# Optimization experiments

Measured on AMD Instinct MI355X. Metric: run time of the kernel, lower is better.

Reference implementation:

```python
import jax, jax.numpy as jnp
import numpy as np

B, T, C = 4, 1024, 1024
H, D = 16, 64


def setup_inputs() -> dict:
    key = jax.random.key(0)
    ks = jax.random.split(key, 5)
    sc = 0.02
    x = jax.random.normal(ks[0], (B, T, C), dtype=jnp.float32)
    Wq = jax.random.normal(ks[1], (H, C, D), dtype=jnp.float32) * sc
    Wk = jax.random.normal(ks[2], (H, C, D), dtype=jnp.float32) * sc
    Wv = jax.random.normal(ks[3], (H, C, D), dtype=jnp.float32) * sc
    Wp = jax.random.normal(ks[4], (H * D, C), dtype=jnp.float32) * sc
    bp = jnp.zeros((C,), dtype=jnp.float32)
    return {"x": x, "Wq": Wq, "Wk": Wk, "Wv": Wv, "Wp": Wp, "bp": bp}


def reference(x, Wq, Wk, Wv, Wp, bp):
    # per-head projections (bias-free, as in nanoGPT Head)
    q = jnp.einsum('btc,hcd->bhtd', x, Wq)
    k = jnp.einsum('btc,hcd->bhtd', x, Wk)
    v = jnp.einsum('btc,hcd->bhtd', x, Wv)
    scale = 1.0 / jnp.sqrt(jnp.asarray(D, dtype=x.dtype))
    scores = jnp.einsum('bhtd,bhsd->bhts', q, k) * scale  # [B,H,T,T]
    causal = jnp.tril(jnp.ones((T, T), dtype=bool))
    scores = jnp.where(causal, scores, jnp.asarray(-jnp.inf, dtype=scores.dtype))
    attn = jax.nn.softmax(scores, axis=-1)
    out = jnp.einsum('bhts,bhsd->bhtd', attn, v)  # [B,H,T,D]
    out = out.transpose(0, 2, 1, 3).reshape(B, T, H * D)  # concat heads
    return out @ Wp + bp  # final projection (dropout=0)
```

## Files before the change

kernel.cpp:

```cpp
#include <hip/hip_runtime.h>
#include <hip/hip_bf16.h>

typedef unsigned short u16;
typedef __bf16 bf16x8 __attribute__((ext_vector_type(8)));
typedef float floatx4 __attribute__((ext_vector_type(4)));

#define SB 4
#define ST 1024
#define SC 1024
#define SH 16
#define SD 64

__device__ __forceinline__ u16 f2bf(float f) {
    unsigned int u = __builtin_bit_cast(unsigned int, f);
    u += 0x7fffu + ((u >> 16) & 1u);
    return (u16)(u >> 16);
}

__device__ __forceinline__ void gload16(const u16* g, u16* l) {
    __builtin_amdgcn_global_load_lds(
        (const __attribute__((address_space(1))) unsigned int*)g,
        (__attribute__((address_space(3))) unsigned int*)l, 16, 0, 0);
}

__global__ void k_prep(const float* __restrict__ x,
                       const float* __restrict__ Wq, const float* __restrict__ Wk,
                       const float* __restrict__ Wv, const float* __restrict__ Wp,
                       u16* __restrict__ xb, u16* __restrict__ Wqkv, u16* __restrict__ Wpt) {
    __shared__ float tile[64 * 65];
    const int id = blockIdx.x, tid = threadIdx.x;
    if (id < 4096) {
        int i = id * 256 + tid;
        float4 v = ((const float4*)x)[i];
        uint2 o;
        o.x = (unsigned)f2bf(v.x) | ((unsigned)f2bf(v.y) << 16);
        o.y = (unsigned)f2bf(v.z) | ((unsigned)f2bf(v.w) << 16);
        ((uint2*)xb)[i] = o;
    } else if (id < 4864) {
        const int id1 = id - 4096;
        const int qkv = id1 >> 8, rem = id1 & 255, h = rem >> 4, c0 = (rem & 15) * 64;
        const float* src = qkv == 0 ? Wq : (qkv == 1 ? Wk : Wv);
        #pragma unroll
        for (int i = 0; i < 16; ++i) {
            int idx = tid + i * 256;
            int r = idx >> 6, d = idx & 63;
            tile[r * 65 + d] = src[(h * SC + c0 + r) * SD + d];
        }
        __syncthreads();
        #pragma unroll
        for (int i = 0; i < 16; ++i) {
            int idx = tid + i * 256;
            int d = idx >> 6, cc = idx & 63;
            Wqkv[(qkv * 1024 + h * SD + d) * SC + c0 + cc] = f2bf(tile[cc * 65 + d]);
        }
    } else {
        const int id2 = id - 4864;
        const int n0 = (id2 & 15) * 64, k0 = (id2 >> 4) * 64;
        #pragma unroll
        for (int i = 0; i < 16; ++i) {
            int idx = tid + i * 256;
            int r = idx >> 6, nn = idx & 63;
            tile[r * 65 + nn] = Wp[(k0 + r) * SC + n0 + nn];
        }
        __syncthreads();
        #pragma unroll
        for (int i = 0; i < 16; ++i) {
            int idx = tid + i * 256;
            int nr = idx >> 6, kk = idx & 63;
            Wpt[(n0 + nr) * (SH * SD) + k0 + kk] = f2bf(tile[kk * 65 + nr]);
        }
    }
}

__launch_bounds__(256)
__global__ void k_gemm(const u16* __restrict__ A, const u16* __restrict__ Bt,
                       int M, int N, int K,
                       u16* __restrict__ Qb, u16* __restrict__ Kb, u16* __restrict__ Vt) {
    constexpr int BM = 128, BN = 128, SM = 4, SN = 4;
    __shared__ u16 Als[BM * 64];
    __shared__ u16 Bls[BN * 64];
    const int tid = threadIdx.x, lane = tid & 63, w = tid >> 6;
    const int quad = lane >> 4, l16 = lane & 15;
    const int sr = lane >> 3, sc = lane & 7;
    const int nt = N / BN;
    const int m0 = (blockIdx.x / nt) * BM, n0 = (blockIdx.x % nt) * BN;
    const int wm = (w >> 1) * 64, wn = (w & 1) * 64;

    floatx4 acc[SM][SN] = {};
    const int niter = K / 64;
    for (int it = 0; it < niter; ++it) {
        const int k0 = it * 64;
        #pragma unroll
        for (int i = 0; i < 4; ++i) {
            int rb = (w * 4 + i) * 8;
            gload16(&A[(long)(m0 + rb + sr) * K + k0 + ((sc ^ sr) << 3)], &Als[rb * 64]);
            gload16(&Bt[(long)(n0 + rb + sr) * K + k0 + ((sc ^ sr) << 3)], &Bls[rb * 64]);
        }
        __syncthreads();
        bf16x8 af[SM][2], bfr[SN][2];
        #pragma unroll
        for (int sm = 0; sm < SM; ++sm) {
            int row = wm + sm * 16 + l16;
            #pragma unroll
            for (int ks = 0; ks < 2; ++ks)
                af[sm][ks] = *(const bf16x8*)&Als[row * 64 + (((ks * 4 + quad) ^ (row & 7)) << 3)];
        }
        #pragma unroll
        for (int sn = 0; sn < SN; ++sn) {
            int row = wn + sn * 16 + l16;
            #pragma unroll
            for (int ks = 0; ks < 2; ++ks)
                bfr[sn][ks] = *(const bf16x8*)&Bls[row * 64 + (((ks * 4 + quad) ^ (row & 7)) << 3)];
        }
        #pragma unroll
        for (int ks = 0; ks < 2; ++ks)
            #pragma unroll
            for (int sm = 0; sm < SM; ++sm)
                #pragma unroll
                for (int sn = 0; sn < SN; ++sn)
                    acc[sm][sn] = __builtin_amdgcn_mfma_f32_16x16x32_bf16(bfr[sn][ks], af[sm][ks], acc[sm][sn], 0, 0, 0);
        if (it + 1 < niter) __syncthreads();
    }
    const int qkv = n0 >> 10;
    const float qs = qkv == 0 ? 0.18033688011112042f : 1.0f;
    #pragma unroll
    for (int sm = 0; sm < SM; ++sm) {
        const int m = m0 + wm + sm * 16 + l16;
        const int bb = m >> 10, t = m & 1023;
        #pragma unroll
        for (int sn = 0; sn < SN; ++sn) {
            const int dl = (n0 & 1023) + wn + sn * 16 + (quad << 2);
            const int h = dl >> 6, d0 = dl & 63;
            u16 pk[4];
            #pragma unroll
            for (int r = 0; r < 4; ++r) pk[r] = f2bf(acc[sm][sn][r] * qs);
            if (qkv == 2) {
                const long vb = (long)(bb * SH + h) * SD * ST + t;
                #pragma unroll
                for (int r = 0; r < 4; ++r) Vt[vb + (long)(d0 + r) * ST] = pk[r];
            } else {
                u16* dst = qkv == 0 ? Qb : Kb;
                *(uint2*)&dst[(((long)(bb * SH + h) * ST + t) << 6) + d0] = *(uint2*)pk;
            }
        }
    }
}

__launch_bounds__(256)
__global__ void k_oproj(const u16* __restrict__ A, const u16* __restrict__ Bt,
                        const float* __restrict__ bias, float* __restrict__ Cout) {
    constexpr int K = 1024, N = 1024;
    __shared__ u16 Als[4][64 * 64];
    __shared__ u16 Bls[4][64 * 64];
    const int tid = threadIdx.x, lane = tid & 63, w = tid >> 6;
    const int quad = lane >> 4, l16 = lane & 15;
    const int sr = lane >> 3, sc = lane & 7;
    const int m0 = (blockIdx.x >> 4) * 64, n0 = (blockIdx.x & 15) * 64;
    const int wm = (w >> 1) * 32, wn = (w & 1) * 32;

    floatx4 acc[2][2] = {};
    for (int kb = 0; kb < 4; ++kb) {
        const int k0 = kb * 256;
        #pragma unroll
        for (int seg = 0; seg < 4; ++seg) {
            #pragma unroll
            for (int i = 0; i < 2; ++i) {
                int rb = (w * 2 + i) * 8;
                gload16(&A[(long)(m0 + rb + sr) * K + k0 + seg * 64 + ((sc ^ sr) << 3)], &Als[seg][rb * 64]);
                gload16(&Bt[(long)(n0 + rb + sr) * K + k0 + seg * 64 + ((sc ^ sr) << 3)], &Bls[seg][rb * 64]);
            }
        }
        __syncthreads();
        #pragma unroll
        for (int seg = 0; seg < 4; ++seg) {
            bf16x8 af[2][2], bfr[2][2];
            #pragma unroll
            for (int sm = 0; sm < 2; ++sm) {
                int row = wm + sm * 16 + l16;
                #pragma unroll
                for (int ks = 0; ks < 2; ++ks)
                    af[sm][ks] = *(const bf16x8*)&Als[seg][row * 64 + (((ks * 4 + quad) ^ (row & 7)) << 3)];
            }
            #pragma unroll
            for (int sn = 0; sn < 2; ++sn) {
                int row = wn + sn * 16 + l16;
                #pragma unroll
                for (int ks = 0; ks < 2; ++ks)
                    bfr[sn][ks] = *(const bf16x8*)&Bls[seg][row * 64 + (((ks * 4 + quad) ^ (row & 7)) << 3)];
            }
            #pragma unroll
            for (int ks = 0; ks < 2; ++ks)
                #pragma unroll
                for (int sm = 0; sm < 2; ++sm)
                    #pragma unroll
                    for (int sn = 0; sn < 2; ++sn)
                        acc[sm][sn] = __builtin_amdgcn_mfma_f32_16x16x32_bf16(bfr[sn][ks], af[sm][ks], acc[sm][sn], 0, 0, 0);
        }
        if (kb < 3) __syncthreads();
    }
    #pragma unroll
    for (int sn = 0; sn < 2; ++sn) {
        const int nb = n0 + wn + sn * 16 + (quad << 2);
        const float4 bv = *(const float4*)&bias[nb];
        #pragma unroll
        for (int sm = 0; sm < 2; ++sm) {
            const int m = m0 + wm + sm * 16 + l16;
            float4 o;
            o.x = acc[sm][sn][0] + bv.x;
            o.y = acc[sm][sn][1] + bv.y;
            o.z = acc[sm][sn][2] + bv.z;
            o.w = acc[sm][sn][3] + bv.w;
            *(float4*)&Cout[(long)m * N + nb] = o;
        }
    }
}

__launch_bounds__(256)
__global__ void k_attn(const u16* __restrict__ Qg, const u16* __restrict__ Kg,
                       const u16* __restrict__ Vtg, u16* __restrict__ Og) {
    __shared__ u16 Kls[2][64 * 64];
    __shared__ u16 Vls[2][64 * 64];
    __shared__ u16 Pls[64 * 64];
    const int tid = threadIdx.x, lane = tid & 63, w = tid >> 6;
    const int quad = lane >> 4, l16 = lane & 15;
    const int sr = lane >> 3, sc = lane & 7;
    const int tile = 15 - (blockIdx.x >> 6);
    const int bh = blockIdx.x & 63;
    const int t0 = tile * 64;
    const int b = bh >> 4, h = bh & 15;
    const u16* Qbh = Qg + (long)bh * ST * SD;
    const u16* Kbh = Kg + (long)bh * ST * SD;
    const u16* Vbh = Vtg + (long)bh * SD * ST;

    bf16x8 qf[2];
    {
        const u16* qrow = Qbh + (t0 + w * 16 + l16) * SD;
        qf[0] = *(const bf16x8*)&qrow[quad * 8];
        qf[1] = *(const bf16x8*)&qrow[32 + quad * 8];
    }
    floatx4 oacc[4] = {};
    float lsum = 0.f;
    const int myt = t0 + w * 16 + l16;
    const int rowP = w * 16 + l16;

    auto stage = [&](int buf, int s0) {
        #pragma unroll
        for (int i = 0; i < 2; ++i) {
            int rb = (w * 2 + i) * 8;
            gload16(&Kbh[(s0 + rb + sr) * SD + ((sc ^ sr) << 3)], &Kls[buf][rb * 64]);
            gload16(&Vbh[(rb + sr) * ST + s0 + ((sc ^ sr) << 3)], &Vls[buf][rb * 64]);
        }
    };

    stage(0, 0);
    for (int j = 0; j <= tile; ++j) {
        const int buf = j & 1;
        const int s0 = j * 64;
        __syncthreads();
        if (j < tile) stage(buf ^ 1, s0 + 64);

        floatx4 sa[4] = {};
        #pragma unroll
        for (int sn = 0; sn < 4; ++sn) {
            int row = sn * 16 + l16;
            #pragma unroll
            for (int ks = 0; ks < 2; ++ks) {
                bf16x8 kf = *(const bf16x8*)&Kls[buf][row * 64 + (((ks * 4 + quad) ^ (row & 7)) << 3)];
                sa[sn] = __builtin_amdgcn_mfma_f32_16x16x32_bf16(kf, qf[ks], sa[sn], 0, 0, 0);
            }
        }
        const bool diag = (j == tile);
        #pragma unroll
        for (int sn = 0; sn < 4; ++sn) {
            const int sl = sn * 16 + (quad << 2);
            u16 pk[4];
            #pragma unroll
            for (int r = 0; r < 4; ++r) {
                float e = __builtin_exp2f(sa[sn][r]);
                if (diag && s0 + sl + r > myt) e = 0.f;
                lsum += e;
                pk[r] = (u16)(__builtin_bit_cast(unsigned int, e) >> 16);
            }
            *(uint2*)&Pls[rowP * 64 + (((sl >> 3) ^ (rowP & 7)) << 3) + ((quad & 1) << 2)] = *(uint2*)pk;
        }
        bf16x8 pf[2];
        #pragma unroll
        for (int ks = 0; ks < 2; ++ks)
            pf[ks] = *(const bf16x8*)&Pls[rowP * 64 + (((ks * 4 + quad) ^ (rowP & 7)) << 3)];
        #pragma unroll
        for (int dn = 0; dn < 4; ++dn) {
            int row = dn * 16 + l16;
            #pragma unroll
            for (int ks = 0; ks < 2; ++ks) {
                bf16x8 vf = *(const bf16x8*)&Vls[buf][row * 64 + (((ks * 4 + quad) ^ (row & 7)) << 3)];
                oacc[dn] = __builtin_amdgcn_mfma_f32_16x16x32_bf16(vf, pf[ks], oacc[dn], 0, 0, 0);
            }
        }
    }
    float l = lsum;
    l += __shfl_xor(l, 16);
    l += __shfl_xor(l, 32);
    const float inv = 1.0f / l;
    const long obase = ((long)(b * ST + myt) << 10) + h * SD;
    #pragma unroll
    for (int dn = 0; dn < 4; ++dn) {
        u16 pk[4];
        #pragma unroll
        for (int r = 0; r < 4; ++r) pk[r] = f2bf(oacc[dn][r] * inv);
        *(uint2*)&Og[obase + dn * 16 + (quad << 2)] = *(uint2*)pk;
    }
}

extern "C" void kernel_launch(void* const* d_in, const int* in_sizes, int n_in,
                              void* d_out, int out_size, void* d_ws, size_t ws_size,
                              hipStream_t stream) {
    const float* x  = (const float*)d_in[0];
    const float* Wq = (const float*)d_in[1];
    const float* Wk = (const float*)d_in[2];
    const float* Wv = (const float*)d_in[3];
    const float* Wp = (const float*)d_in[4];
    const float* bp = (const float*)d_in[5];
    float* out = (float*)d_out;

    char* ws = (char*)d_ws;
    u16* xb   = (u16*)(ws);
    u16* Wqkv = (u16*)(ws + (8ll  << 20));
    u16* Wpt  = (u16*)(ws + (14ll << 20));
    u16* Qb   = (u16*)(ws + (16ll << 20));
    u16* Kb   = (u16*)(ws + (24ll << 20));
    u16* Vt   = (u16*)(ws + (32ll << 20));
    u16* Ob   = (u16*)(ws + (40ll << 20));

    k_prep<<<5120, 256, 0, stream>>>(x, Wq, Wk, Wv, Wp, xb, Wqkv, Wpt);
    k_gemm<<<32 * 24, 256, 0, stream>>>(xb, Wqkv, 4096, 3072, 1024, Qb, Kb, Vt);
    k_attn<<<1024, 256, 0, stream>>>(Qb, Kb, Vt, Ob);
    k_oproj<<<1024, 256, 0, stream>>>(Ob, Wpt, bp, out);
}
```

Measured before the change: 172.2 us.

## Rewrite QKV GEMM with 256x256 tiles and double-buffered async LDS prefetch

Each block of the QKV projection GEMM now computes a 256x256 tile with 512 threads, so the launch drops to 192 blocks. The kernel double-buffers A and B tiles in LDS. Async global-to-LDS loads for the next K steps are issued between the MFMA phases, paced with vmcnt waits and barriers, and MFMA priority is raised with setprio. The goal is more operand reuse per tile and hiding global load latency behind compute. The trade-off is a small grid that leaves many CUs idle, plus much higher LDS and register use per block.

```diff
diff --git a/kernel.cpp b/kernel.cpp
--- a/kernel.cpp
+++ b/kernel.cpp
@@ -72,68 +72,100 @@
     }
 }
 
-__launch_bounds__(256)
+__launch_bounds__(512, 1)
 __global__ void k_gemm(const u16* __restrict__ A, const u16* __restrict__ Bt,
-                       int M, int N, int K,
                        u16* __restrict__ Qb, u16* __restrict__ Kb, u16* __restrict__ Vt) {
-    constexpr int BM = 128, BN = 128, SM = 4, SN = 4;
-    __shared__ u16 Als[BM * 64];
-    __shared__ u16 Bls[BN * 64];
+    constexpr int K = 1024;
+    __shared__ u16 As[2][2][128 * 64];
+    __shared__ u16 Bs[2][2][128 * 64];
     const int tid = threadIdx.x, lane = tid & 63, w = tid >> 6;
     const int quad = lane >> 4, l16 = lane & 15;
     const int sr = lane >> 3, sc = lane & 7;
-    const int nt = N / BN;
-    const int m0 = (blockIdx.x / nt) * BM, n0 = (blockIdx.x % nt) * BN;
-    const int wm = (w >> 1) * 64, wn = (w & 1) * 64;
-
-    floatx4 acc[SM][SN] = {};
-    const int niter = K / 64;
-    for (int it = 0; it < niter; ++it) {
-        const int k0 = it * 64;
-        #pragma unroll
-        for (int i = 0; i < 4; ++i) {
-            int rb = (w * 4 + i) * 8;
-            gload16(&A[(long)(m0 + rb + sr) * K + k0 + ((sc ^ sr) << 3)], &Als[rb * 64]);
-            gload16(&Bt[(long)(n0 + rb + sr) * K + k0 + ((sc ^ sr) << 3)], &Bls[rb * 64]);
-        }
-        __syncthreads();
-        bf16x8 af[SM][2], bfr[SN][2];
-        #pragma unroll
-        for (int sm = 0; sm < SM; ++sm) {
-            int row = wm + sm * 16 + l16;
+    const int m0 = (blockIdx.x / 12) * 256, n0 = (blockIdx.x % 12) * 256;
+    const int wm = (w >> 2) * 128, wn = (w & 3) * 64;
+    const int ah = w >> 2;
+
+    auto stA = [&](int buf, int half, int kt) {
+        #pragma unroll
+        for (int i = 0; i < 2; ++i) {
+            int rb = (w * 2 + i) * 8;
+            gload16(&A[(long)(m0 + half * 128 + rb + sr) * K + kt * 64 + ((sc ^ sr) << 3)],
+                    &As[buf][half][rb * 64]);
+        }
+    };
+    auto stB = [&](int buf, int half, int kt) {
+        #pragma unroll
+        for (int i = 0; i < 2; ++i) {
+            int rb = (w * 2 + i) * 8;
+            gload16(&Bt[(long)(n0 + half * 128 + rb + sr) * K + kt * 64 + ((sc ^ sr) << 3)],
+                    &Bs[buf][half][rb * 64]);
+        }
+    };
+
+    floatx4 acc[8][4] = {};
+    stA(0, 0, 0); stA(0, 1, 0); stB(0, 0, 0); stB(0, 1, 0); stB(1, 0, 1); stB(1, 1, 1);
+    asm volatile("s_waitcnt vmcnt(4)" ::: "memory");
+    __builtin_amdgcn_s_barrier();
+
+    for (int kt = 0; kt < 16; ++kt) {
+        const int buf = kt & 1;
+        bf16x8 bfr[4][2];
+        #pragma unroll
+        for (int q = 0; q < 4; ++q) {
+            if (q == 0) {
+                #pragma unroll
+                for (int nf = 0; nf < 4; ++nf) {
+                    int bn = wn + nf * 16 + l16;
+                    int bh = bn >> 7, r7 = bn & 127;
+                    #pragma unroll
+                    for (int ks = 0; ks < 2; ++ks)
+                        bfr[nf][ks] = *(const bf16x8*)&Bs[buf][bh][r7 * 64 + (((ks * 4 + quad) ^ (r7 & 7)) << 3)];
+                }
+            }
+            bf16x8 af[2][2];
+            #pragma unroll
+            for (int j = 0; j < 2; ++j) {
+                int r7 = (2 * q + j) * 16 + l16;
+                #pragma unroll
+                for (int ks = 0; ks < 2; ++ks)
+                    af[j][ks] = *(const bf16x8*)&As[buf][ah][r7 * 64 + (((ks * 4 + quad) ^ (r7 & 7)) << 3)];
+            }
+            if (q == 0) { if (kt + 1 < 16) stA(buf ^ 1, 0, kt + 1); }
+            else if (q == 1) { if (kt + 1 < 16) stA(buf ^ 1, 1, kt + 1); }
+            else if (q == 2) { if (kt + 2 < 16) stB(buf, 0, kt + 2); }
+            else             { if (kt + 2 < 16) stB(buf, 1, kt + 2); }
+            __builtin_amdgcn_s_barrier();
+            __builtin_amdgcn_s_setprio(1);
             #pragma unroll
             for (int ks = 0; ks < 2; ++ks)
-                af[sm][ks] = *(const bf16x8*)&Als[row * 64 + (((ks * 4 + quad) ^ (row & 7)) << 3)];
-        }
-        #pragma unroll
-        for (int sn = 0; sn < SN; ++sn) {
-            int row = wn + sn * 16 + l16;
-            #pragma unroll
-            for (int ks = 0; ks < 2; ++ks)
-                bfr[sn][ks] = *(const bf16x8*)&Bls[row * 64 + (((ks * 4 + quad) ^ (row & 7)) << 3)];
-        }
-        #pragma unroll
-        for (int ks = 0; ks < 2; ++ks)
-            #pragma unroll
-            for (int sm = 0; sm < SM; ++sm)
-                #pragma unroll
-                for (int sn = 0; sn < SN; ++sn)
-                    acc[sm][sn] = __builtin_amdgcn_mfma_f32_16x16x32_bf16(bfr[sn][ks], af[sm][ks], acc[sm][sn], 0, 0, 0);
-        if (it + 1 < niter) __syncthreads();
-    }
+                #pragma unroll
+                for (int j = 0; j < 2; ++j)
+                    #pragma unroll
+                    for (int nf = 0; nf < 4; ++nf)
+                        acc[2 * q + j][nf] = __builtin_amdgcn_mfma_f32_16x16x32_bf16(
+                            bfr[nf][ks], af[j][ks], acc[2 * q + j][nf], 0, 0, 0);
+            __builtin_amdgcn_s_setprio(0);
+            if (q == 3) {
+                if (kt == 14) asm volatile("s_waitcnt vmcnt(0)" ::: "memory");
+                else          asm volatile("s_waitcnt vmcnt(4)" ::: "memory");
+            }
+            __builtin_amdgcn_s_barrier();
+        }
+    }
+
     const int qkv = n0 >> 10;
     const float qs = qkv == 0 ? 0.18033688011112042f : 1.0f;
     #pragma unroll
-    for (int sm = 0; sm < SM; ++sm) {
-        const int m = m0 + wm + sm * 16 + l16;
-        const int bb = m >> 10, t = m & 1023;
-        #pragma unroll
-        for (int sn = 0; sn < SN; ++sn) {
-            const int dl = (n0 & 1023) + wn + sn * 16 + (quad << 2);
-            const int h = dl >> 6, d0 = dl & 63;
+    for (int nf = 0; nf < 4; ++nf) {
+        const int dl = (n0 & 1023) + wn + nf * 16 + (quad << 2);
+        const int h = dl >> 6, d0 = dl & 63;
+        #pragma unroll
+        for (int mf = 0; mf < 8; ++mf) {
+            const int m = m0 + wm + mf * 16 + l16;
+            const int bb = m >> 10, t = m & 1023;
             u16 pk[4];
             #pragma unroll
-            for (int r = 0; r < 4; ++r) pk[r] = f2bf(acc[sm][sn][r] * qs);
+            for (int r = 0; r < 4; ++r) pk[r] = f2bf(acc[mf][nf][r] * qs);
             if (qkv == 2) {
                 const long vb = (long)(bb * SH + h) * SD * ST + t;
                 #pragma unroll
@@ -332,7 +364,7 @@
     u16* Ob   = (u16*)(ws + (40ll << 20));
 
     k_prep<<<5120, 256, 0, stream>>>(x, Wq, Wk, Wv, Wp, xb, Wqkv, Wpt);
-    k_gemm<<<32 * 24, 256, 0, stream>>>(xb, Wqkv, 4096, 3072, 1024, Qb, Kb, Vt);
+    k_gemm<<<192, 512, 0, stream>>>(xb, Wqkv, Qb, Kb, Vt);
     k_attn<<<1024, 256, 0, stream>>>(Qb, Kb, Vt, Ob);
     k_oproj<<<1024, 256, 0, stream>>>(Ob, Wpt, bp, out);
 }
```

Measured after the change: 174.1 us. About the same (+1.1%).
